# Performance work log

Measured on AMD Instinct MI355X. Metric: run time of the kernel, lower is better.

The kernel has to match this reference:

```python
import jax, jax.numpy as jnp
import numpy as np

OUTPUT_SIZE = 512


def _build_schedule(n, m):
    """Static pyramid-circuit schedule of Givens/RBS gates on n wires.

    Sequential gate order (matches theta ordering): for k = 1..n-1, apply
    gates on adjacent wire pairs (i, i+1) for i = k-1 down to max(k-m, 0).
    Total gates = (2n - m - 1) * m // 2. Gates are packed into a brickwork
    schedule (timestep t = 2(k-1) - i) so each layer touches disjoint pairs
    and the whole chain runs in T = n + m - 2 parallel layers.
    Padded slots point at dummy wires (n, n+1) and are masked to identity.
    """
    layers = {}
    t_idx = 0
    for k in range(1, n):
        for i in range(k - 1, max(k - m, 0) - 1, -1):
            t = 2 * (k - 1) - i
            layers.setdefault(t, []).append((i, t_idx))
            t_idx += 1
    T = max(layers) + 1
    W = max(len(v) for v in layers.values())
    wire = np.full((T, W), n, dtype=np.int32)   # pad gates hit dummy wires (n, n+1)
    tidx = np.zeros((T, W), dtype=np.int32)
    mask = np.zeros((T, W), dtype=np.float32)
    for t, gs in layers.items():
        for j, (i, ti) in enumerate(gs):
            wire[t, j] = i
            tidx[t, j] = ti
            mask[t, j] = 1.0
    return wire, tidx, mask


def apply_orthogonal(thetas, x, output_size):
    input_size = x.shape[-1]
    n, m = max(input_size, output_size), min(input_size, output_size)
    wire, tidx, mask = _build_schedule(n, m)
    if input_size < n:
        x = jnp.pad(x, ((0, 0), (0, n - input_size)))
    state = jnp.pad(x, ((0, 0), (0, 2)))          # two dummy columns for padded gate slots
    th = thetas[jnp.asarray(tidx)]                # [T, W]
    msk = jnp.asarray(mask)
    cos = jnp.where(msk > 0, jnp.cos(th), 1.0)    # padded slots -> identity rotation
    sin = jnp.where(msk > 0, jnp.sin(th), 0.0)
    wa = jnp.asarray(wire)                        # [T, W] first wire of each pair
    wb = wa + 1

    def step(st, layer):
        c, s, a_idx, b_idx = layer
        a = st[:, a_idx]                          # [B, W]
        b = st[:, b_idx]
        st = st.at[:, a_idx].set(c * a + s * b)   # RBS rotation on each pair
        st = st.at[:, b_idx].set(c * b - s * a)
        return st, None

    state, _ = jax.lax.scan(step, state, (cos, sin, wa, wb))
    return state[:, :output_size]


def setup_inputs():
    key = jax.random.key(0)
    k1, k2 = jax.random.split(key)
    B, N = 256, 512
    n_thetas = (2 * max(N, OUTPUT_SIZE) - min(N, OUTPUT_SIZE) - 1) * min(N, OUTPUT_SIZE) // 2
    x = jax.random.normal(k1, (B, N), dtype=jnp.float32)
    thetas = jax.random.uniform(k2, (n_thetas,), dtype=jnp.float32,
                                minval=-np.pi, maxval=np.pi)
    bias = jnp.zeros((OUTPUT_SIZE,), dtype=jnp.float32)
    return {"x": x, "thetas": thetas, "bias": bias}


def reference(x, thetas, bias):
    # normalize_inputs=False path; with_bias=True
    out = apply_orthogonal(thetas, x, OUTPUT_SIZE)
    return out + bias
```

## Files before the change

kernel.cpp:

```cpp
#include <hip/hip_runtime.h>
#include <stdint.h>


#define N_WIRES 512
#define BATCH   256
#define PAIRS   510
#define PF      10
#define FINAL4  (PAIRS * 256)
#define TOTAL4  (FINAL4 + 128)
#define TOTAL2  (TOTAL4 * 2)
#define N_THETAS 130816

__global__ __launch_bounds__(256) void sc_kernel(
    const float* __restrict__ thetas, float2* __restrict__ SC) {
  int tid = blockIdx.x * 256 + threadIdx.x;
  if (tid >= N_THETAS) return;
  float c, s;
  __sincosf(thetas[tid], &s, &c);
  SC[tid] = make_float2(c, s);
}

__global__ __launch_bounds__(256) void build_kernel(
    const float2* __restrict__ SC, float2* __restrict__ W2) {
  int tid = blockIdx.x * 256 + threadIdx.x;
  if (tid >= TOTAL2) return;
  int p = tid >> 9, r = tid & 511;
  int q = r >> 7, L = (r >> 1) & 63, e = r & 1, h = q >> 1;
  int t = 2 * p + h;
  int i = 8 * L + 4 * (q & 1) + 2 * e + h;
  float c = 1.0f, s = 0.0f;
  if (i <= min(t, 1020 - t)) {
    int k = ((t + i) >> 1) + 1;
    int idx = ((k * (k - 1)) >> 1) + (k - 1 - i);
    float2 cs = SC[idx];
    c = cs.x; s = cs.y;
  }
  if (q == 3 && e == 1) c -= 1.0f;
  W2[tid] = make_float2(c, s);
}

__global__ __launch_bounds__(256) void fused_kernel(
    const float* __restrict__ thetas, float2* __restrict__ W2) {
  int tid = blockIdx.x * 256 + threadIdx.x;
  if (tid >= TOTAL2) return;
  int p = tid >> 9, r = tid & 511;
  int q = r >> 7, L = (r >> 1) & 63, e = r & 1, h = q >> 1;
  int t = 2 * p + h;
  int i = 8 * L + 4 * (q & 1) + 2 * e + h;
  float c = 1.0f, s = 0.0f;
  if (i <= min(t, 1020 - t)) {
    int k = ((t + i) >> 1) + 1;
    int idx = ((k * (k - 1)) >> 1) + (k - 1 - i);
    __sincosf(thetas[idx], &s, &c);
  }
  if (q == 3 && e == 1) c -= 1.0f;
  W2[tid] = make_float2(c, s);
}

template <int N>
__device__ __forceinline__ void wait_vm() {
  asm volatile("s_waitcnt vmcnt(%0)" ::"i"(N) : "memory");
}

__device__ __forceinline__ float dpp_shr1(float v) {
  return __int_as_float(
      __builtin_amdgcn_mov_dpp(__float_as_int(v), 0x138, 0xF, 0xF, true));
}
__device__ __forceinline__ float dpp_shl1(float v) {
  return __int_as_float(
      __builtin_amdgcn_mov_dpp(__float_as_int(v), 0x130, 0xF, 0xF, true));
}

__device__ __forceinline__ float2 gate_pk(float2 cs, float2 ab) {
  float2 t, r;
  asm("v_pk_mul_f32 %0, %1, %2 op_sel:[1,1] op_sel_hi:[1,0] neg_hi:[1,0]"
      : "=v"(t)
      : "v"(cs), "v"(ab));
  asm("v_pk_fma_f32 %0, %1, %2, %3 op_sel:[0,0,0] op_sel_hi:[0,1,1]"
      : "=v"(r)
      : "v"(cs), "v"(ab), "v"(t));
  return r;
}

__device__ __forceinline__ void gate_s(float& a, float& b, float c, float s) {
  float na = fmaf(c, a, s * b);
  float nb = fmaf(c, b, -(s * a));
  a = na;
  b = nb;
}

__device__ __forceinline__ void pair_compute(float2& A, float2& B, float2& C,
                                             float2& D, const float4& q0,
                                             const float4& q1, const float4& q2,
                                             const float4& q3) {
  A = gate_pk(make_float2(q0.x, q0.y), A);
  B = gate_pk(make_float2(q0.z, q0.w), B);
  C = gate_pk(make_float2(q1.x, q1.y), C);
  D = gate_pk(make_float2(q1.z, q1.w), D);
  float cl_m1 = dpp_shr1(q3.z);
  float sl    = dpp_shr1(q3.w);
  float rv0 = dpp_shl1(A.x);
  float lv7 = dpp_shr1(D.y);
  gate_s(A.y, B.x, q2.x, q2.y);
  gate_s(B.y, C.x, q2.z, q2.w);
  gate_s(C.y, D.x, q3.x, q3.y);
  float nv7 = fmaf(q3.w, rv0, fmaf(q3.z, D.y, D.y));
  float nv0 = fmaf(-sl, lv7, fmaf(cl_m1, A.x, A.x));
  D.y = nv7;
  A.x = nv0;
}

__global__ __launch_bounds__(64, 1) void circuit_kernel(
    const float* __restrict__ x, const float* __restrict__ W,
    const float* __restrict__ bias, float* __restrict__ out) {
  const int lane = threadIdx.x;
  const int row = blockIdx.x;
  const float4* __restrict__ Wg = (const float4*)W;

  const float* xr = x + row * N_WIRES + lane * 8;
  float4 x0 = *(const float4*)(xr);
  float4 x1 = *(const float4*)(xr + 4);

  float4 R[PF][4];
  const float4* pw = Wg + lane;
#pragma unroll
  for (int s = 0; s < PF; ++s) {
    R[s][0] = pw[0];
    R[s][1] = pw[64];
    R[s][2] = pw[128];
    R[s][3] = pw[192];
    pw += 256;
  }

  float2 A = make_float2(x0.x, x0.y), B = make_float2(x0.z, x0.w);
  float2 C = make_float2(x1.x, x1.y), D = make_float2(x1.z, x1.w);

  for (int blk = 0; blk < (PAIRS / PF) - 1; ++blk) {
#pragma unroll
    for (int s = 0; s < PF; ++s) {
      wait_vm<36>();
      pair_compute(A, B, C, D, R[s][0], R[s][1], R[s][2], R[s][3]);
      R[s][0] = pw[0];
      R[s][1] = pw[64];
      R[s][2] = pw[128];
      R[s][3] = pw[192];
      pw += 256;
    }
  }

  wait_vm<0>();
#pragma unroll
  for (int s = 0; s < PF; ++s)
    pair_compute(A, B, C, D, R[s][0], R[s][1], R[s][2], R[s][3]);

  float4 f0 = Wg[FINAL4 + lane];
  float4 f1 = Wg[FINAL4 + 64 + lane];
  A = gate_pk(make_float2(f0.x, f0.y), A);
  B = gate_pk(make_float2(f0.z, f0.w), B);
  C = gate_pk(make_float2(f1.x, f1.y), C);
  D = gate_pk(make_float2(f1.z, f1.w), D);

  const float* br = bias + lane * 8;
  float4 b0 = *(const float4*)(br);
  float4 b1 = *(const float4*)(br + 4);
  float4 o0 = {A.x + b0.x, A.y + b0.y, B.x + b0.z, B.y + b0.w};
  float4 o1 = {C.x + b1.x, C.y + b1.y, D.x + b1.z, D.y + b1.w};
  float* orow = out + row * N_WIRES + lane * 8;
  *(float4*)(orow) = o0;
  *(float4*)(orow + 4) = o1;
}

extern "C" void kernel_launch(void* const* d_in, const int* in_sizes, int n_in,
                              void* d_out, int out_size, void* d_ws,
                              size_t ws_size, hipStream_t stream) {
  const float* x = (const float*)d_in[0];
  const float* thetas = (const float*)d_in[1];
  const float* bias = (const float*)d_in[2];
  float* out = (float*)d_out;

  float* W = (float*)d_ws;
  size_t table_bytes = (size_t)TOTAL4 * 16;
  size_t sc_bytes = (size_t)N_THETAS * 8;

  if (ws_size >= table_bytes + sc_bytes) {
    float2* SC = (float2*)((char*)d_ws + table_bytes);
    sc_kernel<<<(N_THETAS + 255) / 256, 256, 0, stream>>>(thetas, SC);
    build_kernel<<<(TOTAL2 + 255) / 256, 256, 0, stream>>>(SC, (float2*)W);
  } else {
    fused_kernel<<<(TOTAL2 + 255) / 256, 256, 0, stream>>>(thetas, (float2*)W);
  }
  circuit_kernel<<<BATCH, 64, 0, stream>>>(x, W, bias, out);
}
```

Baseline: 114.9 us.

## Process two batch rows per wave and always use fused sincos table build

Each 64-lane circuit block now carries two batch rows, sharing every loaded gate coefficient across both rows. This halves the coefficient-table traffic per row and gives two independent dependency chains to hide latency, at the cost of launching only 128 blocks on a large GPU. The precompute path also drops the separate sincos and build kernels in favour of the single fused kernel, removing one launch and the intermediate buffer.

```diff
diff --git a/kernel.cpp b/kernel.cpp
--- a/kernel.cpp
+++ b/kernel.cpp
@@ -9,35 +9,6 @@
 #define FINAL4  (PAIRS * 256)
 #define TOTAL4  (FINAL4 + 128)
 #define TOTAL2  (TOTAL4 * 2)
-#define N_THETAS 130816
-
-__global__ __launch_bounds__(256) void sc_kernel(
-    const float* __restrict__ thetas, float2* __restrict__ SC) {
-  int tid = blockIdx.x * 256 + threadIdx.x;
-  if (tid >= N_THETAS) return;
-  float c, s;
-  __sincosf(thetas[tid], &s, &c);
-  SC[tid] = make_float2(c, s);
-}
-
-__global__ __launch_bounds__(256) void build_kernel(
-    const float2* __restrict__ SC, float2* __restrict__ W2) {
-  int tid = blockIdx.x * 256 + threadIdx.x;
-  if (tid >= TOTAL2) return;
-  int p = tid >> 9, r = tid & 511;
-  int q = r >> 7, L = (r >> 1) & 63, e = r & 1, h = q >> 1;
-  int t = 2 * p + h;
-  int i = 8 * L + 4 * (q & 1) + 2 * e + h;
-  float c = 1.0f, s = 0.0f;
-  if (i <= min(t, 1020 - t)) {
-    int k = ((t + i) >> 1) + 1;
-    int idx = ((k * (k - 1)) >> 1) + (k - 1 - i);
-    float2 cs = SC[idx];
-    c = cs.x; s = cs.y;
-  }
-  if (q == 3 && e == 1) c -= 1.0f;
-  W2[tid] = make_float2(c, s);
-}
 
 __global__ __launch_bounds__(256) void fused_kernel(
     const float* __restrict__ thetas, float2* __restrict__ W2) {
@@ -114,12 +85,8 @@
     const float* __restrict__ x, const float* __restrict__ W,
     const float* __restrict__ bias, float* __restrict__ out) {
   const int lane = threadIdx.x;
-  const int row = blockIdx.x;
+  const int row0 = blockIdx.x * 2;
   const float4* __restrict__ Wg = (const float4*)W;
-
-  const float* xr = x + row * N_WIRES + lane * 8;
-  float4 x0 = *(const float4*)(xr);
-  float4 x1 = *(const float4*)(xr + 4);
 
   float4 R[PF][4];
   const float4* pw = Wg + lane;
@@ -132,14 +99,22 @@
     pw += 256;
   }
 
-  float2 A = make_float2(x0.x, x0.y), B = make_float2(x0.z, x0.w);
-  float2 C = make_float2(x1.x, x1.y), D = make_float2(x1.z, x1.w);
+  const float* xr0 = x + row0 * N_WIRES + lane * 8;
+  float4 x0a = *(const float4*)(xr0);
+  float4 x0b = *(const float4*)(xr0 + 4);
+  float4 x1a = *(const float4*)(xr0 + N_WIRES);
+  float4 x1b = *(const float4*)(xr0 + N_WIRES + 4);
+  float2 A0 = make_float2(x0a.x, x0a.y), B0 = make_float2(x0a.z, x0a.w);
+  float2 C0 = make_float2(x0b.x, x0b.y), D0 = make_float2(x0b.z, x0b.w);
+  float2 A1 = make_float2(x1a.x, x1a.y), B1 = make_float2(x1a.z, x1a.w);
+  float2 C1 = make_float2(x1b.x, x1b.y), D1 = make_float2(x1b.z, x1b.w);
 
   for (int blk = 0; blk < (PAIRS / PF) - 1; ++blk) {
 #pragma unroll
     for (int s = 0; s < PF; ++s) {
       wait_vm<36>();
-      pair_compute(A, B, C, D, R[s][0], R[s][1], R[s][2], R[s][3]);
+      pair_compute(A0, B0, C0, D0, R[s][0], R[s][1], R[s][2], R[s][3]);
+      pair_compute(A1, B1, C1, D1, R[s][0], R[s][1], R[s][2], R[s][3]);
       R[s][0] = pw[0];
       R[s][1] = pw[64];
       R[s][2] = pw[128];
@@ -150,24 +125,35 @@
 
   wait_vm<0>();
 #pragma unroll
-  for (int s = 0; s < PF; ++s)
-    pair_compute(A, B, C, D, R[s][0], R[s][1], R[s][2], R[s][3]);
+  for (int s = 0; s < PF; ++s) {
+    pair_compute(A0, B0, C0, D0, R[s][0], R[s][1], R[s][2], R[s][3]);
+    pair_compute(A1, B1, C1, D1, R[s][0], R[s][1], R[s][2], R[s][3]);
+  }
 
   float4 f0 = Wg[FINAL4 + lane];
   float4 f1 = Wg[FINAL4 + 64 + lane];
-  A = gate_pk(make_float2(f0.x, f0.y), A);
-  B = gate_pk(make_float2(f0.z, f0.w), B);
-  C = gate_pk(make_float2(f1.x, f1.y), C);
-  D = gate_pk(make_float2(f1.z, f1.w), D);
+  A0 = gate_pk(make_float2(f0.x, f0.y), A0);
+  B0 = gate_pk(make_float2(f0.z, f0.w), B0);
+  C0 = gate_pk(make_float2(f1.x, f1.y), C0);
+  D0 = gate_pk(make_float2(f1.z, f1.w), D0);
+  A1 = gate_pk(make_float2(f0.x, f0.y), A1);
+  B1 = gate_pk(make_float2(f0.z, f0.w), B1);
+  C1 = gate_pk(make_float2(f1.x, f1.y), C1);
+  D1 = gate_pk(make_float2(f1.z, f1.w), D1);
 
   const float* br = bias + lane * 8;
   float4 b0 = *(const float4*)(br);
   float4 b1 = *(const float4*)(br + 4);
-  float4 o0 = {A.x + b0.x, A.y + b0.y, B.x + b0.z, B.y + b0.w};
-  float4 o1 = {C.x + b1.x, C.y + b1.y, D.x + b1.z, D.y + b1.w};
-  float* orow = out + row * N_WIRES + lane * 8;
-  *(float4*)(orow) = o0;
-  *(float4*)(orow + 4) = o1;
+  float* orow0 = out + row0 * N_WIRES + lane * 8;
+  float4 o00 = {A0.x + b0.x, A0.y + b0.y, B0.x + b0.z, B0.y + b0.w};
+  float4 o01 = {C0.x + b1.x, C0.y + b1.y, D0.x + b1.z, D0.y + b1.w};
+  *(float4*)(orow0) = o00;
+  *(float4*)(orow0 + 4) = o01;
+  float* orow1 = orow0 + N_WIRES;
+  float4 o10 = {A1.x + b0.x, A1.y + b0.y, B1.x + b0.z, B1.y + b0.w};
+  float4 o11 = {C1.x + b1.x, C1.y + b1.y, D1.x + b1.z, D1.y + b1.w};
+  *(float4*)(orow1) = o10;
+  *(float4*)(orow1 + 4) = o11;
 }
 
 extern "C" void kernel_launch(void* const* d_in, const int* in_sizes, int n_in,
@@ -179,15 +165,7 @@
   float* out = (float*)d_out;
 
   float* W = (float*)d_ws;
-  size_t table_bytes = (size_t)TOTAL4 * 16;
-  size_t sc_bytes = (size_t)N_THETAS * 8;
 
-  if (ws_size >= table_bytes + sc_bytes) {
-    float2* SC = (float2*)((char*)d_ws + table_bytes);
-    sc_kernel<<<(N_THETAS + 255) / 256, 256, 0, stream>>>(thetas, SC);
-    build_kernel<<<(TOTAL2 + 255) / 256, 256, 0, stream>>>(SC, (float2*)W);
-  } else {
-    fused_kernel<<<(TOTAL2 + 255) / 256, 256, 0, stream>>>(thetas, (float2*)W);
-  }
-  circuit_kernel<<<BATCH, 64, 0, stream>>>(x, W, bias, out);
+  fused_kernel<<<(TOTAL2 + 255) / 256, 256, 0, stream>>>(thetas, (float2*)W);
+  circuit_kernel<<<BATCH / 2, 64, 0, stream>>>(x, W, bias, out);
 }
```

After: 132.5 us. 15.3% more time.

## Share gate table across four batch rows via LDS double-buffered chunks

Applied to the files above, without the earlier changes.

The circuit kernel now runs four waves per block, one batch row each. All four waves cooperatively stream the gate coefficient table into double-buffered shared memory using global_load_lds, replacing per-wave register prefetch from global memory. This cuts global and L2 traffic for the table fourfold, at the cost of a block barrier per chunk and only 64 blocks on the device. The host path is also simplified to always use the fused sincos/build kernel instead of the two-kernel split.

```diff
diff --git a/kernel.cpp b/kernel.cpp
--- a/kernel.cpp
+++ b/kernel.cpp
@@ -5,39 +5,12 @@
 #define N_WIRES 512
 #define BATCH   256
 #define PAIRS   510
-#define PF      10
+#define CHUNK   6
+#define NCHUNK  85
+#define CHUNK4  (CHUNK * 4 * 64)
 #define FINAL4  (PAIRS * 256)
 #define TOTAL4  (FINAL4 + 128)
 #define TOTAL2  (TOTAL4 * 2)
-#define N_THETAS 130816
-
-__global__ __launch_bounds__(256) void sc_kernel(
-    const float* __restrict__ thetas, float2* __restrict__ SC) {
-  int tid = blockIdx.x * 256 + threadIdx.x;
-  if (tid >= N_THETAS) return;
-  float c, s;
-  __sincosf(thetas[tid], &s, &c);
-  SC[tid] = make_float2(c, s);
-}
-
-__global__ __launch_bounds__(256) void build_kernel(
-    const float2* __restrict__ SC, float2* __restrict__ W2) {
-  int tid = blockIdx.x * 256 + threadIdx.x;
-  if (tid >= TOTAL2) return;
-  int p = tid >> 9, r = tid & 511;
-  int q = r >> 7, L = (r >> 1) & 63, e = r & 1, h = q >> 1;
-  int t = 2 * p + h;
-  int i = 8 * L + 4 * (q & 1) + 2 * e + h;
-  float c = 1.0f, s = 0.0f;
-  if (i <= min(t, 1020 - t)) {
-    int k = ((t + i) >> 1) + 1;
-    int idx = ((k * (k - 1)) >> 1) + (k - 1 - i);
-    float2 cs = SC[idx];
-    c = cs.x; s = cs.y;
-  }
-  if (q == 3 && e == 1) c -= 1.0f;
-  W2[tid] = make_float2(c, s);
-}
 
 __global__ __launch_bounds__(256) void fused_kernel(
     const float* __restrict__ thetas, float2* __restrict__ W2) {
@@ -110,48 +83,53 @@
   A.x = nv0;
 }
 
-__global__ __launch_bounds__(64, 1) void circuit_kernel(
+__device__ __forceinline__ void issue_chunk(const float4* __restrict__ Wg,
+                                            float4* smem, int c, int bsel,
+                                            int wave, int lane) {
+  const float4* src = Wg + c * (CHUNK * 256) + wave * (6 * 64) + lane;
+  float4* dst = smem + bsel * CHUNK4 + wave * (6 * 64);
+#pragma unroll
+  for (int j = 0; j < 6; ++j) {
+    __builtin_amdgcn_global_load_lds(
+        (__attribute__((address_space(1))) uint32_t*)(src + j * 64),
+        (__attribute__((address_space(3))) uint32_t*)(dst + j * 64),
+        16, 0, 0);
+  }
+}
+
+__global__ __launch_bounds__(256, 1) void circuit_kernel(
     const float* __restrict__ x, const float* __restrict__ W,
     const float* __restrict__ bias, float* __restrict__ out) {
-  const int lane = threadIdx.x;
-  const int row = blockIdx.x;
+  __shared__ float4 smem[2 * CHUNK4];
+  const int lane = threadIdx.x & 63;
+  const int wave = threadIdx.x >> 6;
+  const int row = blockIdx.x * 4 + wave;
   const float4* __restrict__ Wg = (const float4*)W;
 
   const float* xr = x + row * N_WIRES + lane * 8;
   float4 x0 = *(const float4*)(xr);
   float4 x1 = *(const float4*)(xr + 4);
-
-  float4 R[PF][4];
-  const float4* pw = Wg + lane;
-#pragma unroll
-  for (int s = 0; s < PF; ++s) {
-    R[s][0] = pw[0];
-    R[s][1] = pw[64];
-    R[s][2] = pw[128];
-    R[s][3] = pw[192];
-    pw += 256;
-  }
-
   float2 A = make_float2(x0.x, x0.y), B = make_float2(x0.z, x0.w);
   float2 C = make_float2(x1.x, x1.y), D = make_float2(x1.z, x1.w);
 
-  for (int blk = 0; blk < (PAIRS / PF) - 1; ++blk) {
+  issue_chunk(Wg, smem, 0, 0, wave, lane);
+  wait_vm<0>();
+  __syncthreads();
+
+  for (int k = 0; k < NCHUNK; ++k) {
+    if (k + 1 < NCHUNK) issue_chunk(Wg, smem, k + 1, (k + 1) & 1, wave, lane);
+    const float4* buf = smem + (k & 1) * CHUNK4;
 #pragma unroll
-    for (int s = 0; s < PF; ++s) {
-      wait_vm<36>();
-      pair_compute(A, B, C, D, R[s][0], R[s][1], R[s][2], R[s][3]);
-      R[s][0] = pw[0];
-      R[s][1] = pw[64];
-      R[s][2] = pw[128];
-      R[s][3] = pw[192];
-      pw += 256;
+    for (int pr = 0; pr < CHUNK; ++pr) {
+      float4 q0 = buf[(pr * 4 + 0) * 64 + lane];
+      float4 q1 = buf[(pr * 4 + 1) * 64 + lane];
+      float4 q2 = buf[(pr * 4 + 2) * 64 + lane];
+      float4 q3 = buf[(pr * 4 + 3) * 64 + lane];
+      pair_compute(A, B, C, D, q0, q1, q2, q3);
     }
+    wait_vm<0>();
+    __syncthreads();
   }
-
-  wait_vm<0>();
-#pragma unroll
-  for (int s = 0; s < PF; ++s)
-    pair_compute(A, B, C, D, R[s][0], R[s][1], R[s][2], R[s][3]);
 
   float4 f0 = Wg[FINAL4 + lane];
   float4 f1 = Wg[FINAL4 + 64 + lane];
@@ -163,9 +141,9 @@
   const float* br = bias + lane * 8;
   float4 b0 = *(const float4*)(br);
   float4 b1 = *(const float4*)(br + 4);
+  float* orow = out + row * N_WIRES + lane * 8;
   float4 o0 = {A.x + b0.x, A.y + b0.y, B.x + b0.z, B.y + b0.w};
   float4 o1 = {C.x + b1.x, C.y + b1.y, D.x + b1.z, D.y + b1.w};
-  float* orow = out + row * N_WIRES + lane * 8;
   *(float4*)(orow) = o0;
   *(float4*)(orow + 4) = o1;
 }
@@ -179,15 +157,7 @@
   float* out = (float*)d_out;
 
   float* W = (float*)d_ws;
-  size_t table_bytes = (size_t)TOTAL4 * 16;
-  size_t sc_bytes = (size_t)N_THETAS * 8;
 
-  if (ws_size >= table_bytes + sc_bytes) {
-    float2* SC = (float2*)((char*)d_ws + table_bytes);
-    sc_kernel<<<(N_THETAS + 255) / 256, 256, 0, stream>>>(thetas, SC);
-    build_kernel<<<(TOTAL2 + 255) / 256, 256, 0, stream>>>(SC, (float2*)W);
-  } else {
-    fused_kernel<<<(TOTAL2 + 255) / 256, 256, 0, stream>>>(thetas, (float2*)W);
-  }
-  circuit_kernel<<<BATCH, 64, 0, stream>>>(x, W, bias, out);
+  fused_kernel<<<(TOTAL2 + 255) / 256, 256, 0, stream>>>(thetas, (float2*)W);
+  circuit_kernel<<<BATCH / 4, 256, 0, stream>>>(x, W, bias, out);
 }
```

Result: slower. 157.3 us (+36.9%).

## Store gate cos/sin table as half2 and use single fused table-build kernel

Applied to the files above, without the earlier changes.

Gate coefficients are now stored as packed fp16 (half2) rather than float2, with a new table layout. This halves the per-lane coefficient stream the circuit kernel loads each step, and the prefetch wait count is adjusted to match. The launch path drops the separate sincos and build kernels in favour of the fused builder. The cost is fp16 rounding of cos/sin across roughly a thousand chained rotations, which may break the numerical tolerance, plus extra half-to-float conversions in the inner loop.

```diff
diff --git a/kernel.cpp b/kernel.cpp
--- a/kernel.cpp
+++ b/kernel.cpp
@@ -1,4 +1,5 @@
 #include <hip/hip_runtime.h>
+#include <hip/hip_fp16.h>
 #include <stdint.h>
 
 
@@ -6,55 +7,32 @@
 #define BATCH   256
 #define PAIRS   510
 #define PF      10
-#define FINAL4  (PAIRS * 256)
-#define TOTAL4  (FINAL4 + 128)
-#define TOTAL2  (TOTAL4 * 2)
-#define N_THETAS 130816
-
-__global__ __launch_bounds__(256) void sc_kernel(
-    const float* __restrict__ thetas, float2* __restrict__ SC) {
-  int tid = blockIdx.x * 256 + threadIdx.x;
-  if (tid >= N_THETAS) return;
-  float c, s;
-  __sincosf(thetas[tid], &s, &c);
-  SC[tid] = make_float2(c, s);
-}
-
-__global__ __launch_bounds__(256) void build_kernel(
-    const float2* __restrict__ SC, float2* __restrict__ W2) {
-  int tid = blockIdx.x * 256 + threadIdx.x;
-  if (tid >= TOTAL2) return;
-  int p = tid >> 9, r = tid & 511;
-  int q = r >> 7, L = (r >> 1) & 63, e = r & 1, h = q >> 1;
-  int t = 2 * p + h;
-  int i = 8 * L + 4 * (q & 1) + 2 * e + h;
-  float c = 1.0f, s = 0.0f;
-  if (i <= min(t, 1020 - t)) {
-    int k = ((t + i) >> 1) + 1;
-    int idx = ((k * (k - 1)) >> 1) + (k - 1 - i);
-    float2 cs = SC[idx];
-    c = cs.x; s = cs.y;
-  }
-  if (q == 3 && e == 1) c -= 1.0f;
-  W2[tid] = make_float2(c, s);
-}
+#define FINAL4  (PAIRS * 128)
+#define TOTAL4  (FINAL4 + 64)
+#define TOTALH2 (TOTAL4 * 4)
 
 __global__ __launch_bounds__(256) void fused_kernel(
-    const float* __restrict__ thetas, float2* __restrict__ W2) {
+    const float* __restrict__ thetas, __half2* __restrict__ Wh) {
   int tid = blockIdx.x * 256 + threadIdx.x;
-  if (tid >= TOTAL2) return;
-  int p = tid >> 9, r = tid & 511;
-  int q = r >> 7, L = (r >> 1) & 63, e = r & 1, h = q >> 1;
-  int t = 2 * p + h;
-  int i = 8 * L + 4 * (q & 1) + 2 * e + h;
+  if (tid >= TOTALH2) return;
   float c = 1.0f, s = 0.0f;
-  if (i <= min(t, 1020 - t)) {
-    int k = ((t + i) >> 1) + 1;
-    int idx = ((k * (k - 1)) >> 1) + (k - 1 - i);
-    __sincosf(thetas[idx], &s, &c);
+  if (tid < PAIRS * 512) {
+    int p = tid >> 9, r = tid & 511;
+    int h = r >> 8, rr = r & 255, L = rr >> 2, j = rr & 3;
+    int t = 2 * p + h;
+    int i = 8 * L + 2 * j + h;
+    if (i <= min(t, 1020 - t)) {
+      int k = ((t + i) >> 1) + 1;
+      int idx = ((k * (k - 1)) >> 1) + (k - 1 - i);
+      __sincosf(thetas[idx], &s, &c);
+    }
+    if (h == 1 && j == 3) c -= 1.0f;
+  } else {
+    int e = tid - PAIRS * 512;
+    int L = e >> 2, j = e & 3;
+    if (8 * L + 2 * j == 0) __sincosf(thetas[130815], &s, &c);
   }
-  if (q == 3 && e == 1) c -= 1.0f;
-  W2[tid] = make_float2(c, s);
+  Wh[tid] = __floats2half2_rn(c, s);
 }
 
 template <int N>
@@ -69,6 +47,13 @@
 __device__ __forceinline__ float dpp_shl1(float v) {
   return __int_as_float(
       __builtin_amdgcn_mov_dpp(__float_as_int(v), 0x130, 0xF, 0xF, true));
+}
+__device__ __forceinline__ uint32_t dpp_shr1_u(uint32_t v) {
+  return (uint32_t)__builtin_amdgcn_mov_dpp((int)v, 0x138, 0xF, 0xF, true);
+}
+
+__device__ __forceinline__ float2 h2f(uint32_t u) {
+  return __half22float2(__builtin_bit_cast(__half2, u));
 }
 
 __device__ __forceinline__ float2 gate_pk(float2 cs, float2 ab) {
@@ -90,82 +75,76 @@
 }
 
 __device__ __forceinline__ void pair_compute(float2& A, float2& B, float2& C,
-                                             float2& D, const float4& q0,
-                                             const float4& q1, const float4& q2,
-                                             const float4& q3) {
-  A = gate_pk(make_float2(q0.x, q0.y), A);
-  B = gate_pk(make_float2(q0.z, q0.w), B);
-  C = gate_pk(make_float2(q1.x, q1.y), C);
-  D = gate_pk(make_float2(q1.z, q1.w), D);
-  float cl_m1 = dpp_shr1(q3.z);
-  float sl    = dpp_shr1(q3.w);
+                                             float2& D, const uint4& E,
+                                             const uint4& O) {
+  A = gate_pk(h2f(E.x), A);
+  B = gate_pk(h2f(E.y), B);
+  C = gate_pk(h2f(E.z), C);
+  D = gate_pk(h2f(E.w), D);
+  uint32_t bl = dpp_shr1_u(O.w);
   float rv0 = dpp_shl1(A.x);
   float lv7 = dpp_shr1(D.y);
-  gate_s(A.y, B.x, q2.x, q2.y);
-  gate_s(B.y, C.x, q2.z, q2.w);
-  gate_s(C.y, D.x, q3.x, q3.y);
-  float nv7 = fmaf(q3.w, rv0, fmaf(q3.z, D.y, D.y));
-  float nv0 = fmaf(-sl, lv7, fmaf(cl_m1, A.x, A.x));
+  float2 gl = h2f(bl);
+  float2 gu = h2f(O.w);
+  float2 g4 = h2f(O.x), g5 = h2f(O.y), g6 = h2f(O.z);
+  gate_s(A.y, B.x, g4.x, g4.y);
+  gate_s(B.y, C.x, g5.x, g5.y);
+  gate_s(C.y, D.x, g6.x, g6.y);
+  float nv7 = fmaf(gu.y, rv0, fmaf(gu.x, D.y, D.y));
+  float nv0 = fmaf(-gl.y, lv7, fmaf(gl.x, A.x, A.x));
   D.y = nv7;
   A.x = nv0;
 }
 
 __global__ __launch_bounds__(64, 1) void circuit_kernel(
-    const float* __restrict__ x, const float* __restrict__ W,
+    const float* __restrict__ x, const uint32_t* __restrict__ W,
     const float* __restrict__ bias, float* __restrict__ out) {
   const int lane = threadIdx.x;
   const int row = blockIdx.x;
-  const float4* __restrict__ Wg = (const float4*)W;
+  const uint4* __restrict__ Wg = (const uint4*)W;
+
+  uint4 R[PF][2];
+  const uint4* pw = Wg + lane;
+#pragma unroll
+  for (int s = 0; s < PF; ++s) {
+    R[s][0] = pw[0];
+    R[s][1] = pw[64];
+    pw += 128;
+  }
 
   const float* xr = x + row * N_WIRES + lane * 8;
   float4 x0 = *(const float4*)(xr);
   float4 x1 = *(const float4*)(xr + 4);
-
-  float4 R[PF][4];
-  const float4* pw = Wg + lane;
-#pragma unroll
-  for (int s = 0; s < PF; ++s) {
-    R[s][0] = pw[0];
-    R[s][1] = pw[64];
-    R[s][2] = pw[128];
-    R[s][3] = pw[192];
-    pw += 256;
-  }
-
   float2 A = make_float2(x0.x, x0.y), B = make_float2(x0.z, x0.w);
   float2 C = make_float2(x1.x, x1.y), D = make_float2(x1.z, x1.w);
 
   for (int blk = 0; blk < (PAIRS / PF) - 1; ++blk) {
 #pragma unroll
     for (int s = 0; s < PF; ++s) {
-      wait_vm<36>();
-      pair_compute(A, B, C, D, R[s][0], R[s][1], R[s][2], R[s][3]);
+      wait_vm<18>();
+      pair_compute(A, B, C, D, R[s][0], R[s][1]);
       R[s][0] = pw[0];
       R[s][1] = pw[64];
-      R[s][2] = pw[128];
-      R[s][3] = pw[192];
-      pw += 256;
+      pw += 128;
     }
   }
 
   wait_vm<0>();
 #pragma unroll
-  for (int s = 0; s < PF; ++s)
-    pair_compute(A, B, C, D, R[s][0], R[s][1], R[s][2], R[s][3]);
+  for (int s = 0; s < PF; ++s) pair_compute(A, B, C, D, R[s][0], R[s][1]);
 
-  float4 f0 = Wg[FINAL4 + lane];
-  float4 f1 = Wg[FINAL4 + 64 + lane];
-  A = gate_pk(make_float2(f0.x, f0.y), A);
-  B = gate_pk(make_float2(f0.z, f0.w), B);
-  C = gate_pk(make_float2(f1.x, f1.y), C);
-  D = gate_pk(make_float2(f1.z, f1.w), D);
+  uint4 F = Wg[FINAL4 + lane];
+  A = gate_pk(h2f(F.x), A);
+  B = gate_pk(h2f(F.y), B);
+  C = gate_pk(h2f(F.z), C);
+  D = gate_pk(h2f(F.w), D);
 
   const float* br = bias + lane * 8;
   float4 b0 = *(const float4*)(br);
   float4 b1 = *(const float4*)(br + 4);
+  float* orow = out + row * N_WIRES + lane * 8;
   float4 o0 = {A.x + b0.x, A.y + b0.y, B.x + b0.z, B.y + b0.w};
   float4 o1 = {C.x + b1.x, C.y + b1.y, D.x + b1.z, D.y + b1.w};
-  float* orow = out + row * N_WIRES + lane * 8;
   *(float4*)(orow) = o0;
   *(float4*)(orow + 4) = o1;
 }
@@ -178,16 +157,8 @@
   const float* bias = (const float*)d_in[2];
   float* out = (float*)d_out;
 
-  float* W = (float*)d_ws;
-  size_t table_bytes = (size_t)TOTAL4 * 16;
-  size_t sc_bytes = (size_t)N_THETAS * 8;
+  uint32_t* W = (uint32_t*)d_ws;
 
-  if (ws_size >= table_bytes + sc_bytes) {
-    float2* SC = (float2*)((char*)d_ws + table_bytes);
-    sc_kernel<<<(N_THETAS + 255) / 256, 256, 0, stream>>>(thetas, SC);
-    build_kernel<<<(TOTAL2 + 255) / 256, 256, 0, stream>>>(SC, (float2*)W);
-  } else {
-    fused_kernel<<<(TOTAL2 + 255) / 256, 256, 0, stream>>>(thetas, (float2*)W);
-  }
+  fused_kernel<<<(TOTALH2 + 255) / 256, 256, 0, stream>>>(thetas, (__half2*)W);
   circuit_kernel<<<BATCH, 64, 0, stream>>>(x, W, bias, out);
 }
```

Result: faster. 110.2 us (-4.1%).
